# Kernel tuning notes

Hardware: AMD Instinct MI355X
Metric: run time of the kernel (lower is better)

The kernel has to match this reference:

```python
import jax, jax.numpy as jnp
import numpy as np

EMBED = 768
E2 = EMBED // 2  # 384
B = 128
T = 256   # 16x16 search tokens
T1 = 64   # 8x8 template tokens
EPS = 1e-5


def setup_inputs() -> dict:
    key = jax.random.key(0)
    ks = jax.random.split(key, 8)
    s = 0.02
    return {
        "z_r": jax.random.normal(ks[0], (B, T1, EMBED), jnp.float32),
        "z_i": jax.random.normal(ks[1], (B, T1, EMBED), jnp.float32),
        "x_r": jax.random.normal(ks[2], (B, T, EMBED), jnp.float32),
        "x_i": jax.random.normal(ks[3], (B, T, EMBED), jnp.float32),
        "fz_w": jax.random.normal(ks[4], (E2, 2 * EMBED), jnp.float32) * s,
        "fz_b": jnp.zeros((E2,), jnp.float32),
        "ln_g": jnp.ones((E2,), jnp.float32),
        "ln_b": jnp.zeros((E2,), jnp.float32),
        "wr": jax.random.normal(ks[5], (E2, EMBED, 3, 3), jnp.float32) * s,
        "br": jnp.zeros((E2,), jnp.float32),
        "bnr_g": jnp.ones((E2,), jnp.float32),
        "bnr_b": jnp.zeros((E2,), jnp.float32),
        "bnr_m": jnp.zeros((E2,), jnp.float32),
        "bnr_v": jnp.ones((E2,), jnp.float32),
        "wi": jax.random.normal(ks[6], (E2, EMBED, 3, 3), jnp.float32) * s,
        "bi": jnp.zeros((E2,), jnp.float32),
        "bni_g": jnp.ones((E2,), jnp.float32),
        "bni_b": jnp.zeros((E2,), jnp.float32),
        "bni_m": jnp.zeros((E2,), jnp.float32),
        "bni_v": jnp.ones((E2,), jnp.float32),
        "c": jnp.ones((1,), jnp.float32) * E2,
    }


def _gelu(x):
    return jax.nn.gelu(x, approximate=False)


def _layernorm(x, g, b):
    mu = jnp.mean(x, axis=-1, keepdims=True)
    var = jnp.mean(jnp.square(x - mu), axis=-1, keepdims=True)
    return (x - mu) * jax.lax.rsqrt(var + EPS) * g + b


def _conv_bn_gelu(x, w, b, g, beta, m, v):
    # x: [B, C_in, H, W], w: [C_out, C_in, 3, 3]; BN in eval mode (running stats)
    y = jax.lax.conv_general_dilated(
        x, w, window_strides=(1, 1), padding=((1, 1), (1, 1)),
        dimension_numbers=("NCHW", "OIHW", "NCHW"))
    y = y + b[None, :, None, None]
    y = (y - m[None, :, None, None]) * jax.lax.rsqrt(v[None, :, None, None] + EPS)
    y = y * g[None, :, None, None] + beta[None, :, None, None]
    return _gelu(y)


def _xcorr_fast(x, kernel):
    # x: [B, C, H, W]; kernel: [B, C, kh, kw] -> per-sample valid correlation
    def one(xb, kb):
        return jax.lax.conv_general_dilated(
            xb[None], kb[None], window_strides=(1, 1), padding="VALID",
            dimension_numbers=("NCHW", "OIHW", "NCHW"))[0]
    return jax.vmap(one)(x, kernel)  # [B, 1, oh, ow]


def reference(z_r, z_i, x_r, x_i, fz_w, fz_b, ln_g, ln_b,
              wr, br, bnr_g, bnr_b, bnr_m, bnr_v,
              wi, bi, bni_g, bni_b, bni_m, bni_v, c):
    Bn, t, embed = x_r.shape
    t1 = z_r.shape[1]
    sq, sq1 = int(np.sqrt(t)), int(np.sqrt(t1))
    # f_z: Linear + LayerNorm + GELU on concat(z_r, z_i)
    z = jnp.concatenate((z_r, z_i), axis=2)          # [B, t1, 2*embed]
    z = jnp.einsum("bte,oe->bto", z, fz_w) + fz_b    # [B, t1, E2]
    z = _gelu(_layernorm(z, ln_g, ln_b))
    z_f = z.transpose(0, 2, 1).reshape(Bn, -1, sq1, sq1)  # [B, E2, 8, 8]
    # down_r / down_i on search features
    xr = x_r.transpose(0, 2, 1).reshape(Bn, embed, sq, sq)
    xi = x_i.transpose(0, 2, 1).reshape(Bn, embed, sq, sq)
    xr = _conv_bn_gelu(xr, wr, br, bnr_g, bnr_b, bnr_m, bnr_v)
    xi = _conv_bn_gelu(xi, wi, bi, bni_g, bni_b, bni_m, bni_v)
    # center crop 16x16 -> 8x8
    xr = xr[:, :, 4:-4, 4:-4]
    xi = xi[:, :, 4:-4, 4:-4]
    s1 = jax.nn.sigmoid(_xcorr_fast(xr, z_f) / c)
    s2 = jax.nn.sigmoid(_xcorr_fast(xi, z_f) / c)
    return (s1, s2)
```

## Files before the change

### kernel.cpp

```cpp
#include <hip/hip_runtime.h>
#include <hip/hip_bf16.h>
#include <math.h>

#define EPSF 1e-5f

typedef __bf16 v8bf __attribute__((ext_vector_type(8)));
typedef float  v4f  __attribute__((ext_vector_type(4)));
typedef unsigned int u32;
typedef unsigned short u16;

__device__ __forceinline__ float gelu_exact(float x) {
    return 0.5f * x * (1.0f + erff(x * 0.70710678f));
}
__device__ __forceinline__ u16 f2bf(float f) {
    u32 u = __float_as_uint(f);
    return (u16)((u + 0x7fffu + ((u >> 16) & 1u)) >> 16);
}
__device__ __forceinline__ float bf2f(u16 u) {
    return __uint_as_float(((u32)u) << 16);
}
__device__ __forceinline__ void gload16(const void* g, void* l) {
    __builtin_amdgcn_global_load_lds((const __attribute__((address_space(1))) u32*)g,
                                     (__attribute__((address_space(3))) u32*)l, 16, 0, 0);
}

#define BARRIER(N) do { \
    asm volatile("s_waitcnt vmcnt(" #N ") lgkmcnt(0)" ::: "memory"); \
    __builtin_amdgcn_s_barrier(); \
} while (0)

__global__ __launch_bounds__(256) void kprep_z(const float* __restrict__ fz_w,
                                               u16* __restrict__ Bz) {
    int idx = blockIdx.x * 256 + threadIdx.x;
    int n = idx / 192;
    int r = idx % 192;
    int ec2 = r >> 2;
    int h = r & 3;
    const float* src = fz_w + (size_t)n * 1536 + ec2 * 32 + h * 8;
    float4 v0 = *(const float4*)src;
    float4 v1 = *(const float4*)(src + 4);
    uint4 pk;
    pk.x = (u32)f2bf(v0.x) | ((u32)f2bf(v0.y) << 16);
    pk.y = (u32)f2bf(v0.z) | ((u32)f2bf(v0.w) << 16);
    pk.z = (u32)f2bf(v1.x) | ((u32)f2bf(v1.y) << 16);
    pk.w = (u32)f2bf(v1.z) | ((u32)f2bf(v1.w) << 16);
    size_t slot = ((size_t)(ec2 * 4 + h) * 384 + n);
    *(uint4*)(Bz + slot * 8) = pk;
}

__global__ __launch_bounds__(256) void kprep_w(const float* __restrict__ wr,
                                               const float* __restrict__ wi,
                                               u16* __restrict__ Bw) {
    __shared__ float wsm[6912];
    const int tid = threadIdx.x;
    const int n = blockIdx.x >> 1;
    const int conv = blockIdx.x & 1;
    const float* w = (conv ? wi : wr) + (size_t)n * 6912;
#pragma unroll
    for (int k = 0; k < 7; ++k) {
        int sl = tid + k * 256;
        if (sl < 1728) ((float4*)wsm)[sl] = ((const float4*)w)[sl];
    }
    __syncthreads();
#pragma unroll
    for (int k = 0; k < 4; ++k) {
        int sl = tid + k * 256;
        if (sl < 864) {
            int h = sl & 3;
            int r = sl >> 2;
            int ec2 = r % 24;
            int s = r / 24;
            int ch0 = ec2 * 32 + h * 8;
            u16 tmp[8];
#pragma unroll
            for (int e = 0; e < 8; ++e) tmp[e] = f2bf(wsm[(ch0 + e) * 9 + s]);
            uint4 pk;
            pk.x = (u32)tmp[0] | ((u32)tmp[1] << 16);
            pk.y = (u32)tmp[2] | ((u32)tmp[3] << 16);
            pk.z = (u32)tmp[4] | ((u32)tmp[5] << 16);
            pk.w = (u32)tmp[6] | ((u32)tmp[7] << 16);
            size_t slot = ((size_t)conv * 864 + sl) * 384 + n;
            *(uint4*)(Bw + slot * 8) = pk;
        }
    }
}

#define ZB_BUF 24576
#define ZA_BUF 2048

__global__ __launch_bounds__(384, 1) void kz2(const float* __restrict__ z_r,
                                              const float* __restrict__ z_i,
                                              const u16* __restrict__ Bz,
                                              const float* __restrict__ fz_b,
                                              const float* __restrict__ ln_g,
                                              const float* __restrict__ ln_b,
                                              u16* __restrict__ zpk) {
    const int th = blockIdx.x;
    const int b  = blockIdx.y;
    const int tid  = threadIdx.x;
    const int lane = tid & 63;
    const int wid  = tid >> 6;
    const int l15  = lane & 15;
    const int h    = lane >> 4;

    __shared__ __align__(16) char lds[3 * ZB_BUF + 2 * ZA_BUF];
    char* ldsZB = lds;
    char* ldsZA = lds + 3 * ZB_BUF;
    __shared__ float redS[6 * 32], redQ[6 * 32], mu_s[32], rs_s[32];

    const float* zr_b = z_r + (size_t)b * (64 * 768);
    const float* zi_b = z_i + (size_t)b * (64 * 768);

    int boff[4];
#pragma unroll
    for (int nj = 0; nj < 4; ++nj) {
        int n = wid * 64 + nj * 16 + l15;
        boff[nj] = h * 6144 + n * 16;
    }
    int zaoff[2];
#pragma unroll
    for (int mi = 0; mi < 2; ++mi)
        zaoff[mi] = h * 512 + (mi * 16 + l15) * 16;

    auto stageZB = [&](int ec2, char* buf) {
        const char* src = (const char*)(Bz + (size_t)ec2 * 1536 * 8);
#pragma unroll
        for (int k = 0; k < 4; ++k) {
            int sl = tid + k * 384;
            gload16(src + sl * 16, buf + sl * 16);
        }
    };
    auto issueZA = [&](int ec2, float4* zr) {
        const float* zsrc = (ec2 < 24) ? zr_b : zi_b;
        const int ch0 = (ec2 < 24 ? ec2 : ec2 - 24) * 32;
        int sl = tid & 255;
        int row = sl >> 3, qq = sl & 7;
        zr[0] = *(const float4*)(zsrc + (size_t)(th * 32 + row) * 768 + ch0 + qq * 4);
    };
    auto convertZA = [&](const float4* zr, char* buf) {
        int sl = tid & 255;
        int row = sl >> 3, qq = sl & 7;
        ushort4 pk;
        pk.x = f2bf(zr[0].x); pk.y = f2bf(zr[0].y);
        pk.z = f2bf(zr[0].z); pk.w = f2bf(zr[0].w);
        *(ushort4*)(buf + (qq >> 1) * 512 + row * 16 + (qq & 1) * 8) = pk;
    };

    v4f acc[2][4] = {};

    auto comp = [&](char* curA, char* curB) {
        v8bf a[2], bfv[4];
#pragma unroll
        for (int mi = 0; mi < 2; ++mi) a[mi] = *(const v8bf*)(curA + zaoff[mi]);
#pragma unroll
        for (int nj = 0; nj < 4; ++nj) bfv[nj] = *(const v8bf*)(curB + boff[nj]);
        __builtin_amdgcn_s_setprio(1);
#pragma unroll
        for (int mi = 0; mi < 2; ++mi)
#pragma unroll
            for (int nj = 0; nj < 4; ++nj)
                acc[mi][nj] = __builtin_amdgcn_mfma_f32_16x16x32_bf16(a[mi], bfv[nj], acc[mi][nj], 0, 0, 0);
        __builtin_amdgcn_s_setprio(0);
    };

    float4 zreg[1];
    {
        issueZA(0, zreg);
        stageZB(0, ldsZB);
        stageZB(1, ldsZB + ZB_BUF);
        convertZA(zreg, ldsZA);
        issueZA(1, zreg);
        BARRIER(5);
    }
#pragma unroll 1
    for (int t = 0; t < 46; ++t) {
        stageZB(t + 2, ldsZB + ((t + 2) % 3) * ZB_BUF);
        comp(ldsZA + (t & 1) * ZA_BUF, ldsZB + (t % 3) * ZB_BUF);
        convertZA(zreg, ldsZA + ((t + 1) & 1) * ZA_BUF);
        issueZA(t + 2, zreg);
        BARRIER(5);
    }
    {
        comp(ldsZA + (46 & 1) * ZA_BUF, ldsZB + (46 % 3) * ZB_BUF);
        convertZA(zreg, ldsZA + (47 & 1) * ZA_BUF);
        BARRIER(0);
    }
    comp(ldsZA + (47 & 1) * ZA_BUF, ldsZB + (47 % 3) * ZB_BUF);

    float fzb[4], lng[4], lnb[4];
#pragma unroll
    for (int nj = 0; nj < 4; ++nj) {
        int o = wid * 64 + nj * 16 + l15;
        fzb[nj] = fz_b[o]; lng[nj] = ln_g[o]; lnb[nj] = ln_b[o];
    }
#pragma unroll
    for (int mi = 0; mi < 2; ++mi)
#pragma unroll
        for (int nj = 0; nj < 4; ++nj)
#pragma unroll
            for (int reg = 0; reg < 4; ++reg)
                acc[mi][nj][reg] += fzb[nj];

#pragma unroll
    for (int mi = 0; mi < 2; ++mi) {
#pragma unroll
        for (int reg = 0; reg < 4; ++reg) {
            float s = 0.f, q = 0.f;
#pragma unroll
            for (int nj = 0; nj < 4; ++nj) {
                float v = acc[mi][nj][reg];
                s += v; q += v * v;
            }
#pragma unroll
            for (int m = 0; m < 4; ++m) {
                s += __shfl_xor(s, 1 << m, 64);
                q += __shfl_xor(q, 1 << m, 64);
            }
            if (l15 == 0) {
                int row = mi * 16 + h * 4 + reg;
                redS[wid * 32 + row] = s;
                redQ[wid * 32 + row] = q;
            }
        }
    }
    __syncthreads();
    if (tid < 32) {
        float s = 0.f, q = 0.f;
#pragma unroll
        for (int w6 = 0; w6 < 6; ++w6) { s += redS[w6 * 32 + tid]; q += redQ[w6 * 32 + tid]; }
        float mu = s * (1.0f / 384.0f);
        float var = q * (1.0f / 384.0f) - mu * mu;
        mu_s[tid] = mu;
        rs_s[tid] = rsqrtf(var + EPSF);
    }
    __syncthreads();

#pragma unroll
    for (int mi = 0; mi < 2; ++mi)
#pragma unroll
        for (int nj = 0; nj < 4; ++nj) {
            int o = wid * 64 + nj * 16 + l15;
            u32* dst = (u32*)zpk + ((size_t)b * 384 + o) * 32 + th * 16 + mi * 8 + h * 2;
#pragma unroll
            for (int rp = 0; rp < 2; ++rp) {
                float zv[2];
#pragma unroll
                for (int k = 0; k < 2; ++k) {
                    int reg = rp * 2 + k;
                    int row = mi * 16 + h * 4 + reg;
                    float v = (acc[mi][nj][reg] - mu_s[row]) * rs_s[row] * lng[nj] + lnb[nj];
                    zv[k] = gelu_exact(v);
                }
                dst[rp] = (u32)f2bf(zv[0]) | ((u32)f2bf(zv[1]) << 16);
            }
        }
}

#define APL14  2816
#define ABUF14 (4 * APL14)
#define SSTR14 589824
#define ESTR14 24576

__global__ __launch_bounds__(768, 3) void kc14(const float* __restrict__ x_r,
                                               const float* __restrict__ x_i,
                                               const u16* __restrict__ Bw,
                                               const u16* __restrict__ zpk,
                                               const float* __restrict__ br,  const float* __restrict__ bnr_g,
                                               const float* __restrict__ bnr_b, const float* __restrict__ bnr_m,
                                               const float* __restrict__ bnr_v,
                                               const float* __restrict__ bi,  const float* __restrict__ bni_g,
                                               const float* __restrict__ bni_b, const float* __restrict__ bni_m,
                                               const float* __restrict__ bni_v,
                                               float* __restrict__ part) {
    const int conv = blockIdx.x;
    const int b    = blockIdx.y;
    const int tid  = threadIdx.x;
    const int lane = tid & 63;
    const int wid  = tid >> 6;
    const int l15  = lane & 15;
    const int h    = lane >> 4;

    __shared__ __align__(16) char ldsA[2 * ABUF14];
    __shared__ float redF[12];

    const float* x  = conv ? x_i : x_r;
    const float* xb = x + (size_t)b * (256 * 768);

    const char* bbase = (const char*)(Bw + (size_t)conv * (864 * 384 * 8))
                      + (size_t)h * 6144 + (wid * 32 + l15) * 16;

    int aoff[4];
#pragma unroll
    for (int mi = 0; mi < 4; ++mi) {
        int p = mi * 16 + l15;
        int i = p >> 3, j = p & 7;
        aoff[mi] = h * APL14 + (i * 16 + j + 3) * 16;
    }

    auto issueA = [&](int ec2, float4* ar) {
#pragma unroll
        for (int k = 0; k < 2; ++k) {
            int sl = tid + k * 768;
            if (sl >= 1408) sl -= 1408;
            int row = sl >> 3, qq = sl & 7;
            ar[k] = *(const float4*)(xb + (size_t)(48 + row) * 768 + ec2 * 32 + qq * 4);
        }
    };
    auto convertA = [&](const float4* ar, char* buf) {
#pragma unroll
        for (int k = 0; k < 2; ++k) {
            int sl = tid + k * 768;
            if (sl >= 1408) sl -= 1408;
            int row = sl >> 3, qq = sl & 7;
            ushort4 pk;
            pk.x = f2bf(ar[k].x); pk.y = f2bf(ar[k].y);
            pk.z = f2bf(ar[k].z); pk.w = f2bf(ar[k].w);
            *(ushort4*)(buf + (qq >> 1) * APL14 + row * 16 + (qq & 1) * 8) = pk;
        }
    };

    v4f acc[4][2] = {};
    v8bf bpipe[3][2];
    float4 areg[2];

    {
        issueA(0, areg);
#pragma unroll
        for (int i = 0; i < 3; ++i) {
            const char* p = bbase + (size_t)i * SSTR14;
            bpipe[i][0] = *(const v8bf*)p;
            bpipe[i][1] = *(const v8bf*)(p + 256);
        }
        convertA(areg, ldsA);
        BARRIER(6);
    }

#define TAP(S) do { \
        v8bf b0 = bpipe[(S) % 3][0]; \
        v8bf b1 = bpipe[(S) % 3][1]; \
        const int _so = (((S) / 3) * 16 + ((S) % 3)) * 16; \
        v8bf a0 = *(const v8bf*)(Acur + aoff[0] + _so); \
        v8bf a1 = *(const v8bf*)(Acur + aoff[1] + _so); \
        v8bf a2 = *(const v8bf*)(Acur + aoff[2] + _so); \
        v8bf a3 = *(const v8bf*)(Acur + aoff[3] + _so); \
        __builtin_amdgcn_s_setprio(1); \
        acc[0][0] = __builtin_amdgcn_mfma_f32_16x16x32_bf16(a0, b0, acc[0][0], 0, 0, 0); \
        acc[0][1] = __builtin_amdgcn_mfma_f32_16x16x32_bf16(a0, b1, acc[0][1], 0, 0, 0); \
        acc[1][0] = __builtin_amdgcn_mfma_f32_16x16x32_bf16(a1, b0, acc[1][0], 0, 0, 0); \
        acc[1][1] = __builtin_amdgcn_mfma_f32_16x16x32_bf16(a1, b1, acc[1][1], 0, 0, 0); \
        acc[2][0] = __builtin_amdgcn_mfma_f32_16x16x32_bf16(a2, b0, acc[2][0], 0, 0, 0); \
        acc[2][1] = __builtin_amdgcn_mfma_f32_16x16x32_bf16(a2, b1, acc[2][1], 0, 0, 0); \
        acc[3][0] = __builtin_amdgcn_mfma_f32_16x16x32_bf16(a3, b0, acc[3][0], 0, 0, 0); \
        acc[3][1] = __builtin_amdgcn_mfma_f32_16x16x32_bf16(a3, b1, acc[3][1], 0, 0, 0); \
        __builtin_amdgcn_s_setprio(0); \
        if ((S) <= 5) { \
            const char* _p = bptr + (size_t)((S) + 3) * SSTR14; \
            bpipe[(S) % 3][0] = *(const v8bf*)_p; \
            bpipe[(S) % 3][1] = *(const v8bf*)(_p + 256); \
        } else if (e < 23) { \
            const char* _p = bptr + ESTR14 + (size_t)((S) - 6) * SSTR14; \
            bpipe[(S) % 3][0] = *(const v8bf*)_p; \
            bpipe[(S) % 3][1] = *(const v8bf*)(_p + 256); \
        } \
    } while (0)

#pragma unroll 1
    for (int e = 0; e < 24; ++e) {
        const char* Acur = ldsA + (e & 1) * ABUF14;
        const char* bptr = bbase + (size_t)e * ESTR14;
        TAP(0); TAP(1); TAP(2);
        if (e < 23) issueA(e + 1, areg);
        TAP(3); TAP(4); TAP(5); TAP(6);
        if (e < 23) convertA(areg, ldsA + ((e + 1) & 1) * ABUF14);
        TAP(7); TAP(8);
        if (e < 23) BARRIER(6);
    }
#undef TAP

    const float* bcp = conv ? bi    : br;
    const float* gp  = conv ? bni_g : bnr_g;
    const float* bbp = conv ? bni_b : bnr_b;
    const float* mp  = conv ? bni_m : bnr_m;
    const float* vp  = conv ? bni_v : bnr_v;

    float sum = 0.f;
#pragma unroll
    for (int nj = 0; nj < 2; ++nj) {
        const int o = wid * 32 + nj * 16 + l15;
        const float sc  = gp[o] * rsqrtf(vp[o] + EPSF);
        const float sh2 = (bcp[o] - mp[o]) * sc + bbp[o];
        const u16* zb = zpk + ((size_t)b * 384 + o) * 64;
#pragma unroll
        for (int mi = 0; mi < 4; ++mi) {
            ushort4 zw = *(const ushort4*)(zb + mi * 16 + h * 4);
#pragma unroll
            for (int reg = 0; reg < 4; ++reg) {
                float y = fmaf(acc[mi][nj][reg], sc, sh2);
                u16 zu = (reg == 0) ? zw.x : (reg == 1) ? zw.y : (reg == 2) ? zw.z : zw.w;
                sum = fmaf(gelu_exact(y), bf2f(zu), sum);
            }
        }
    }
#pragma unroll
    for (int off = 32; off >= 1; off >>= 1) sum += __shfl_down(sum, off, 64);

    if (lane == 0) redF[wid] = sum;
    __syncthreads();
    if (tid == 0) {
        float t = 0.f;
#pragma unroll
        for (int w12 = 0; w12 < 12; ++w12) t += redF[w12];
        part[(size_t)conv * 128 + b] = t;
    }
}

__global__ __launch_bounds__(256) void kr(const float* __restrict__ part,
                                          const float* __restrict__ c,
                                          float* __restrict__ out) {
    int v = threadIdx.x;
    out[v] = 1.f / (1.f + expf(-part[v] / c[0]));
}

extern "C" void kernel_launch(void* const* d_in, const int* in_sizes, int n_in,
                              void* d_out, int out_size, void* d_ws, size_t ws_size,
                              hipStream_t stream) {
    const float* z_r   = (const float*)d_in[0];
    const float* z_i   = (const float*)d_in[1];
    const float* x_r   = (const float*)d_in[2];
    const float* x_i   = (const float*)d_in[3];
    const float* fz_w  = (const float*)d_in[4];
    const float* fz_b  = (const float*)d_in[5];
    const float* ln_g  = (const float*)d_in[6];
    const float* ln_b  = (const float*)d_in[7];
    const float* wr    = (const float*)d_in[8];
    const float* br    = (const float*)d_in[9];
    const float* bnr_g = (const float*)d_in[10];
    const float* bnr_b = (const float*)d_in[11];
    const float* bnr_m = (const float*)d_in[12];
    const float* bnr_v = (const float*)d_in[13];
    const float* wi    = (const float*)d_in[14];
    const float* bi    = (const float*)d_in[15];
    const float* bni_g = (const float*)d_in[16];
    const float* bni_b = (const float*)d_in[17];
    const float* bni_m = (const float*)d_in[18];
    const float* bni_v = (const float*)d_in[19];
    const float* c     = (const float*)d_in[20];

    u16*   Bz   = (u16*)d_ws;
    u16*   Bw   = (u16*)((char*)d_ws + 1179648);
    u16*   zpk  = (u16*)((char*)d_ws + 1179648 + 10616832);
    float* part = (float*)((char*)d_ws + 1179648 + 10616832 + 6291456);

    kprep_z<<<288, 256, 0, stream>>>(fz_w, Bz);
    kprep_w<<<768, 256, 0, stream>>>(wr, wi, Bw);
    kz2<<<dim3(2, 128), 384, 0, stream>>>(z_r, z_i, Bz, fz_b, ln_g, ln_b, zpk);
    kc14<<<dim3(2, 128), 768, 0, stream>>>(x_r, x_i, Bw, zpk,
                                           br, bnr_g, bnr_b, bnr_m, bnr_v,
                                           bi, bni_g, bni_b, bni_m, bni_v,
                                           part);
    kr<<<1, 256, 0, stream>>>(part, c, (float*)d_out);
}
```

Baseline: 163.9 us.

## Split conv K loop across two wave groups with wider N tiles per wave

The conv kernel now splits its 12 waves into two groups that each take alternate 32-channel input slabs (split-K), while each wave covers 64 output channels instead of 32. The A slabs for both groups are loaded per iteration, which halves the loop count and the barrier count and gives each A fragment read from LDS twice as many MFMAs. Partial accumulators are combined through LDS at the end, and only group 0 runs the epilogue. This doubles accumulator and B-pipeline register use, which risks spills or lower occupancy, and adds an LDS reduction step.

```diff
diff --git a/kernel.cpp b/kernel.cpp
--- a/kernel.cpp
+++ b/kernel.cpp
@@ -256,12 +256,12 @@
         }
 }
 
-#define APL14  2816
-#define ABUF14 (4 * APL14)
-#define SSTR14 589824
-#define ESTR14 24576
-
-__global__ __launch_bounds__(768, 3) void kc14(const float* __restrict__ x_r,
+#define APL15  2816
+#define SLAB15 (4 * APL15)
+#define SSTR15 589824
+#define ESTR15 24576
+
+__global__ __launch_bounds__(768, 3) void kc15(const float* __restrict__ x_r,
                                                const float* __restrict__ x_i,
                                                const u16* __restrict__ Bw,
                                                const u16* __restrict__ zpk,
@@ -277,140 +277,180 @@
     const int tid  = threadIdx.x;
     const int lane = tid & 63;
     const int wid  = tid >> 6;
+    const int g    = (wid >= 6) ? 1 : 0;
+    const int cg   = wid - g * 6;
     const int l15  = lane & 15;
     const int h    = lane >> 4;
 
-    __shared__ __align__(16) char ldsA[2 * ABUF14];
+    __shared__ __align__(16) char ldsA[4 * SLAB15];
     __shared__ float redF[12];
 
     const float* x  = conv ? x_i : x_r;
     const float* xb = x + (size_t)b * (256 * 768);
 
     const char* bbase = (const char*)(Bw + (size_t)conv * (864 * 384 * 8))
-                      + (size_t)h * 6144 + (wid * 32 + l15) * 16;
+                      + (size_t)h * 6144 + (cg * 64 + l15) * 16;
 
     int aoff[4];
 #pragma unroll
     for (int mi = 0; mi < 4; ++mi) {
         int p = mi * 16 + l15;
         int i = p >> 3, j = p & 7;
-        aoff[mi] = h * APL14 + (i * 16 + j + 3) * 16;
-    }
-
-    auto issueA = [&](int ec2, float4* ar) {
-#pragma unroll
-        for (int k = 0; k < 2; ++k) {
+        aoff[mi] = h * APL15 + (i * 16 + j + 3) * 16;
+    }
+
+    auto issueA = [&](int eBase, float4* ar) {
+#pragma unroll
+        for (int k = 0; k < 4; ++k) {
             int sl = tid + k * 768;
-            if (sl >= 1408) sl -= 1408;
-            int row = sl >> 3, qq = sl & 7;
-            ar[k] = *(const float4*)(xb + (size_t)(48 + row) * 768 + ec2 * 32 + qq * 4);
+            if (sl >= 2816) sl -= 2816;
+            int par = (sl >= 1408) ? 1 : 0;
+            int r2 = sl - par * 1408;
+            int row = r2 >> 3, qq = r2 & 7;
+            ar[k] = *(const float4*)(xb + (size_t)(48 + row) * 768 + (eBase + par) * 32 + qq * 4);
         }
     };
-    auto convertA = [&](const float4* ar, char* buf) {
-#pragma unroll
-        for (int k = 0; k < 2; ++k) {
+    auto convertA = [&](const float4* ar, char* bufBase) {
+#pragma unroll
+        for (int k = 0; k < 4; ++k) {
             int sl = tid + k * 768;
-            if (sl >= 1408) sl -= 1408;
-            int row = sl >> 3, qq = sl & 7;
+            if (sl >= 2816) sl -= 2816;
+            int par = (sl >= 1408) ? 1 : 0;
+            int r2 = sl - par * 1408;
+            int row = r2 >> 3, qq = r2 & 7;
             ushort4 pk;
             pk.x = f2bf(ar[k].x); pk.y = f2bf(ar[k].y);
             pk.z = f2bf(ar[k].z); pk.w = f2bf(ar[k].w);
-            *(ushort4*)(buf + (qq >> 1) * APL14 + row * 16 + (qq & 1) * 8) = pk;
+            *(ushort4*)(bufBase + par * SLAB15 + (qq >> 1) * APL15 + row * 16 + (qq & 1) * 8) = pk;
         }
     };
 
-    v4f acc[4][2] = {};
-    v8bf bpipe[3][2];
-    float4 areg[2];
+    v4f acc[4][4] = {};
+    v8bf bpipe[3][4];
+    float4 areg[4];
 
     {
         issueA(0, areg);
 #pragma unroll
         for (int i = 0; i < 3; ++i) {
-            const char* p = bbase + (size_t)i * SSTR14;
-            bpipe[i][0] = *(const v8bf*)p;
-            bpipe[i][1] = *(const v8bf*)(p + 256);
+            const char* p = bbase + (size_t)g * ESTR15 + (size_t)i * SSTR15;
+#pragma unroll
+            for (int nj = 0; nj < 4; ++nj)
+                bpipe[i][nj] = *(const v8bf*)(p + nj * 256);
         }
         convertA(areg, ldsA);
-        BARRIER(6);
+        BARRIER(12);
     }
 
 #define TAP(S) do { \
-        v8bf b0 = bpipe[(S) % 3][0]; \
-        v8bf b1 = bpipe[(S) % 3][1]; \
         const int _so = (((S) / 3) * 16 + ((S) % 3)) * 16; \
         v8bf a0 = *(const v8bf*)(Acur + aoff[0] + _so); \
         v8bf a1 = *(const v8bf*)(Acur + aoff[1] + _so); \
         v8bf a2 = *(const v8bf*)(Acur + aoff[2] + _so); \
         v8bf a3 = *(const v8bf*)(Acur + aoff[3] + _so); \
         __builtin_amdgcn_s_setprio(1); \
-        acc[0][0] = __builtin_amdgcn_mfma_f32_16x16x32_bf16(a0, b0, acc[0][0], 0, 0, 0); \
-        acc[0][1] = __builtin_amdgcn_mfma_f32_16x16x32_bf16(a0, b1, acc[0][1], 0, 0, 0); \
-        acc[1][0] = __builtin_amdgcn_mfma_f32_16x16x32_bf16(a1, b0, acc[1][0], 0, 0, 0); \
-        acc[1][1] = __builtin_amdgcn_mfma_f32_16x16x32_bf16(a1, b1, acc[1][1], 0, 0, 0); \
-        acc[2][0] = __builtin_amdgcn_mfma_f32_16x16x32_bf16(a2, b0, acc[2][0], 0, 0, 0); \
-        acc[2][1] = __builtin_amdgcn_mfma_f32_16x16x32_bf16(a2, b1, acc[2][1], 0, 0, 0); \
-        acc[3][0] = __builtin_amdgcn_mfma_f32_16x16x32_bf16(a3, b0, acc[3][0], 0, 0, 0); \
-        acc[3][1] = __builtin_amdgcn_mfma_f32_16x16x32_bf16(a3, b1, acc[3][1], 0, 0, 0); \
+        acc[0][0] = __builtin_amdgcn_mfma_f32_16x16x32_bf16(a0, bpipe[(S) % 3][0], acc[0][0], 0, 0, 0); \
+        acc[0][1] = __builtin_amdgcn_mfma_f32_16x16x32_bf16(a0, bpipe[(S) % 3][1], acc[0][1], 0, 0, 0); \
+        acc[0][2] = __builtin_amdgcn_mfma_f32_16x16x32_bf16(a0, bpipe[(S) % 3][2], acc[0][2], 0, 0, 0); \
+        acc[0][3] = __builtin_amdgcn_mfma_f32_16x16x32_bf16(a0, bpipe[(S) % 3][3], acc[0][3], 0, 0, 0); \
+        acc[1][0] = __builtin_amdgcn_mfma_f32_16x16x32_bf16(a1, bpipe[(S) % 3][0], acc[1][0], 0, 0, 0); \
+        acc[1][1] = __builtin_amdgcn_mfma_f32_16x16x32_bf16(a1, bpipe[(S) % 3][1], acc[1][1], 0, 0, 0); \
+        acc[1][2] = __builtin_amdgcn_mfma_f32_16x16x32_bf16(a1, bpipe[(S) % 3][2], acc[1][2], 0, 0, 0); \
+        acc[1][3] = __builtin_amdgcn_mfma_f32_16x16x32_bf16(a1, bpipe[(S) % 3][3], acc[1][3], 0, 0, 0); \
+        acc[2][0] = __builtin_amdgcn_mfma_f32_16x16x32_bf16(a2, bpipe[(S) % 3][0], acc[2][0], 0, 0, 0); \
+        acc[2][1] = __builtin_amdgcn_mfma_f32_16x16x32_bf16(a2, bpipe[(S) % 3][1], acc[2][1], 0, 0, 0); \
+        acc[2][2] = __builtin_amdgcn_mfma_f32_16x16x32_bf16(a2, bpipe[(S) % 3][2], acc[2][2], 0, 0, 0); \
+        acc[2][3] = __builtin_amdgcn_mfma_f32_16x16x32_bf16(a2, bpipe[(S) % 3][3], acc[2][3], 0, 0, 0); \
+        acc[3][0] = __builtin_amdgcn_mfma_f32_16x16x32_bf16(a3, bpipe[(S) % 3][0], acc[3][0], 0, 0, 0); \
+        acc[3][1] = __builtin_amdgcn_mfma_f32_16x16x32_bf16(a3, bpipe[(S) % 3][1], acc[3][1], 0, 0, 0); \
+        acc[3][2] = __builtin_amdgcn_mfma_f32_16x16x32_bf16(a3, bpipe[(S) % 3][2], acc[3][2], 0, 0, 0); \
+        acc[3][3] = __builtin_amdgcn_mfma_f32_16x16x32_bf16(a3, bpipe[(S) % 3][3], acc[3][3], 0, 0, 0); \
         __builtin_amdgcn_s_setprio(0); \
         if ((S) <= 5) { \
-            const char* _p = bptr + (size_t)((S) + 3) * SSTR14; \
+            const char* _p = bptr + (size_t)((S) + 3) * SSTR15; \
             bpipe[(S) % 3][0] = *(const v8bf*)_p; \
             bpipe[(S) % 3][1] = *(const v8bf*)(_p + 256); \
-        } else if (e < 23) { \
-            const char* _p = bptr + ESTR14 + (size_t)((S) - 6) * SSTR14; \
+            bpipe[(S) % 3][2] = *(const v8bf*)(_p + 512); \
+            bpipe[(S) % 3][3] = *(const v8bf*)(_p + 768); \
+        } else if (t < 11) { \
+            const char* _p = bptr + 2 * ESTR15 + (size_t)((S) - 6) * SSTR15; \
             bpipe[(S) % 3][0] = *(const v8bf*)_p; \
             bpipe[(S) % 3][1] = *(const v8bf*)(_p + 256); \
+            bpipe[(S) % 3][2] = *(const v8bf*)(_p + 512); \
+            bpipe[(S) % 3][3] = *(const v8bf*)(_p + 768); \
         } \
     } while (0)
 
 #pragma unroll 1
-    for (int e = 0; e < 24; ++e) {
-        const char* Acur = ldsA + (e & 1) * ABUF14;
-        const char* bptr = bbase + (size_t)e * ESTR14;
+    for (int t = 0; t < 12; ++t) {
+        const char* Acur = ldsA + ((t & 1) * 2 + g) * SLAB15;
+        const char* bptr = bbase + (size_t)(2 * t + g) * ESTR15;
         TAP(0); TAP(1); TAP(2);
-        if (e < 23) issueA(e + 1, areg);
+        if (t < 11) issueA(2 * t + 2, areg);
         TAP(3); TAP(4); TAP(5); TAP(6);
-        if (e < 23) convertA(areg, ldsA + ((e + 1) & 1) * ABUF14);
+        if (t < 11) convertA(areg, ldsA + (((t + 1) & 1) * 2) * SLAB15);
         TAP(7); TAP(8);
-        if (e < 23) BARRIER(6);
+        if (t < 11) BARRIER(12);
     }
 #undef TAP
 
-    const float* bcp = conv ? bi    : br;
-    const float* gp  = conv ? bni_g : bnr_g;
-    const float* bbp = conv ? bni_b : bnr_b;
-    const float* mp  = conv ? bni_m : bnr_m;
-    const float* vp  = conv ? bni_v : bnr_v;
+    __syncthreads();
+    float* P = (float*)ldsA;
+#pragma unroll
+    for (int mi = 0; mi < 4; ++mi) {
+        if (g == 1) {
+#pragma unroll
+            for (int nj = 0; nj < 4; ++nj)
+#pragma unroll
+                for (int reg = 0; reg < 4; ++reg)
+                    P[(((nj * 4 + reg) * 6 + cg) * 64) + lane] = acc[mi][nj][reg];
+        }
+        __syncthreads();
+        if (g == 0) {
+#pragma unroll
+            for (int nj = 0; nj < 4; ++nj)
+#pragma unroll
+                for (int reg = 0; reg < 4; ++reg)
+                    acc[mi][nj][reg] += P[(((nj * 4 + reg) * 6 + cg) * 64) + lane];
+        }
+        __syncthreads();
+    }
 
     float sum = 0.f;
-#pragma unroll
-    for (int nj = 0; nj < 2; ++nj) {
-        const int o = wid * 32 + nj * 16 + l15;
-        const float sc  = gp[o] * rsqrtf(vp[o] + EPSF);
-        const float sh2 = (bcp[o] - mp[o]) * sc + bbp[o];
-        const u16* zb = zpk + ((size_t)b * 384 + o) * 64;
-#pragma unroll
-        for (int mi = 0; mi < 4; ++mi) {
-            ushort4 zw = *(const ushort4*)(zb + mi * 16 + h * 4);
-#pragma unroll
-            for (int reg = 0; reg < 4; ++reg) {
-                float y = fmaf(acc[mi][nj][reg], sc, sh2);
-                u16 zu = (reg == 0) ? zw.x : (reg == 1) ? zw.y : (reg == 2) ? zw.z : zw.w;
-                sum = fmaf(gelu_exact(y), bf2f(zu), sum);
+    if (g == 0) {
+        const float* bcp = conv ? bi    : br;
+        const float* gp  = conv ? bni_g : bnr_g;
+        const float* bbp = conv ? bni_b : bnr_b;
+        const float* mp  = conv ? bni_m : bnr_m;
+        const float* vp  = conv ? bni_v : bnr_v;
+#pragma unroll
+        for (int nj = 0; nj < 4; ++nj) {
+            const int o = cg * 64 + nj * 16 + l15;
+            const float sc  = gp[o] * rsqrtf(vp[o] + EPSF);
+            const float sh2 = (bcp[o] - mp[o]) * sc + bbp[o];
+            const u16* zb = zpk + ((size_t)b * 384 + o) * 64;
+#pragma unroll
+            for (int mi = 0; mi < 4; ++mi) {
+                ushort4 zw = *(const ushort4*)(zb + mi * 16 + h * 4);
+#pragma unroll
+                for (int reg = 0; reg < 4; ++reg) {
+                    float y = fmaf(acc[mi][nj][reg], sc, sh2);
+                    u16 zu = (reg == 0) ? zw.x : (reg == 1) ? zw.y : (reg == 2) ? zw.z : zw.w;
+                    sum = fmaf(gelu_exact(y), bf2f(zu), sum);
+                }
             }
         }
-    }
-#pragma unroll
-    for (int off = 32; off >= 1; off >>= 1) sum += __shfl_down(sum, off, 64);
-
-    if (lane == 0) redF[wid] = sum;
+#pragma unroll
+        for (int off = 32; off >= 1; off >>= 1) sum += __shfl_down(sum, off, 64);
+    }
+
+    if (lane == 0) redF[wid] = (g == 0) ? sum : 0.f;
     __syncthreads();
     if (tid == 0) {
-        float t = 0.f;
-#pragma unroll
-        for (int w12 = 0; w12 < 12; ++w12) t += redF[w12];
-        part[(size_t)conv * 128 + b] = t;
+        float tt = 0.f;
+#pragma unroll
+        for (int w12 = 0; w12 < 12; ++w12) tt += redF[w12];
+        part[(size_t)conv * 128 + b] = tt;
     }
 }
 
@@ -454,7 +494,7 @@
     kprep_z<<<288, 256, 0, stream>>>(fz_w, Bz);
     kprep_w<<<768, 256, 0, stream>>>(wr, wi, Bw);
     kz2<<<dim3(2, 128), 384, 0, stream>>>(z_r, z_i, Bz, fz_b, ln_g, ln_b, zpk);
-    kc14<<<dim3(2, 128), 768, 0, stream>>>(x_r, x_i, Bw, zpk,
+    kc15<<<dim3(2, 128), 768, 0, stream>>>(x_r, x_i, Bw, zpk,
                                            br, bnr_g, bnr_b, bnr_m, bnr_v,
                                            bi, bni_g, bni_b, bni_m, bni_v,
                                            part);
```

New measurement: 245.9 us. 50.0% more time.

## Split conv blocks by output-row halves with wider per-wave channel tiles

Applied to the files above, without the earlier changes.

The conv+xcorr kernel now launches four blocks per batch item, so each (conv, half of the cropped rows) pair gets its own block. Each block has 6 waves, and each wave covers 64 output channels over 32 positions instead of 32 channels over 64 positions. Each block stages a smaller input slab in LDS, and the two partial sums are combined in the final sigmoid kernel. This doubles the grid for better CU occupancy and load balance, but every weight tile is now read by twice as many blocks and each thread holds more B-pipeline registers.

```diff
diff --git a/kernel.cpp b/kernel.cpp
--- a/kernel.cpp
+++ b/kernel.cpp
@@ -256,12 +256,12 @@
         }
 }
 
-#define APL14  2816
-#define ABUF14 (4 * APL14)
-#define SSTR14 589824
-#define ESTR14 24576
-
-__global__ __launch_bounds__(768, 3) void kc14(const float* __restrict__ x_r,
+#define APL16  1536
+#define ABUF16 (4 * APL16)
+#define SSTR16 589824
+#define ESTR16 24576
+
+__global__ __launch_bounds__(384, 3) void kc16(const float* __restrict__ x_r,
                                                const float* __restrict__ x_i,
                                                const u16* __restrict__ Bw,
                                                const u16* __restrict__ zpk,
@@ -272,7 +272,9 @@
                                                const float* __restrict__ bni_b, const float* __restrict__ bni_m,
                                                const float* __restrict__ bni_v,
                                                float* __restrict__ part) {
-    const int conv = blockIdx.x;
+    const int q    = blockIdx.x;
+    const int conv = q >> 1;
+    const int mh   = q & 1;
     const int b    = blockIdx.y;
     const int tid  = threadIdx.x;
     const int lane = tid & 63;
@@ -280,100 +282,99 @@
     const int l15  = lane & 15;
     const int h    = lane >> 4;
 
-    __shared__ __align__(16) char ldsA[2 * ABUF14];
-    __shared__ float redF[12];
+    __shared__ __align__(16) char ldsA[2 * ABUF16];
+    __shared__ float redF[6];
 
     const float* x  = conv ? x_i : x_r;
     const float* xb = x + (size_t)b * (256 * 768);
 
     const char* bbase = (const char*)(Bw + (size_t)conv * (864 * 384 * 8))
-                      + (size_t)h * 6144 + (wid * 32 + l15) * 16;
-
-    int aoff[4];
-#pragma unroll
-    for (int mi = 0; mi < 4; ++mi) {
+                      + (size_t)h * 6144 + (wid * 64 + l15) * 16;
+
+    int aoff[2];
+#pragma unroll
+    for (int mi = 0; mi < 2; ++mi) {
         int p = mi * 16 + l15;
-        int i = p >> 3, j = p & 7;
-        aoff[mi] = h * APL14 + (i * 16 + j + 3) * 16;
+        int li = p >> 3, j = p & 7;
+        aoff[mi] = h * APL16 + (li * 16 + j + 3) * 16;
     }
 
     auto issueA = [&](int ec2, float4* ar) {
 #pragma unroll
         for (int k = 0; k < 2; ++k) {
-            int sl = tid + k * 768;
-            if (sl >= 1408) sl -= 1408;
+            int sl = tid + k * 384;
             int row = sl >> 3, qq = sl & 7;
-            ar[k] = *(const float4*)(xb + (size_t)(48 + row) * 768 + ec2 * 32 + qq * 4);
+            ar[k] = *(const float4*)(xb + (size_t)(48 + mh * 64 + row) * 768 + ec2 * 32 + qq * 4);
         }
     };
     auto convertA = [&](const float4* ar, char* buf) {
 #pragma unroll
         for (int k = 0; k < 2; ++k) {
-            int sl = tid + k * 768;
-            if (sl >= 1408) sl -= 1408;
+            int sl = tid + k * 384;
             int row = sl >> 3, qq = sl & 7;
             ushort4 pk;
             pk.x = f2bf(ar[k].x); pk.y = f2bf(ar[k].y);
             pk.z = f2bf(ar[k].z); pk.w = f2bf(ar[k].w);
-            *(ushort4*)(buf + (qq >> 1) * APL14 + row * 16 + (qq & 1) * 8) = pk;
-        }
-    };
-
-    v4f acc[4][2] = {};
-    v8bf bpipe[3][2];
+            *(ushort4*)(buf + (qq >> 1) * APL16 + row * 16 + (qq & 1) * 8) = pk;
+        }
+    };
+
+    v4f acc[2][4] = {};
+    v8bf bpipe[3][4];
     float4 areg[2];
 
     {
         issueA(0, areg);
 #pragma unroll
         for (int i = 0; i < 3; ++i) {
-            const char* p = bbase + (size_t)i * SSTR14;
-            bpipe[i][0] = *(const v8bf*)p;
-            bpipe[i][1] = *(const v8bf*)(p + 256);
+            const char* p = bbase + (size_t)i * SSTR16;
+#pragma unroll
+            for (int nj = 0; nj < 4; ++nj)
+                bpipe[i][nj] = *(const v8bf*)(p + nj * 256);
         }
         convertA(areg, ldsA);
-        BARRIER(6);
+        BARRIER(12);
     }
 
 #define TAP(S) do { \
-        v8bf b0 = bpipe[(S) % 3][0]; \
-        v8bf b1 = bpipe[(S) % 3][1]; \
         const int _so = (((S) / 3) * 16 + ((S) % 3)) * 16; \
         v8bf a0 = *(const v8bf*)(Acur + aoff[0] + _so); \
         v8bf a1 = *(const v8bf*)(Acur + aoff[1] + _so); \
-        v8bf a2 = *(const v8bf*)(Acur + aoff[2] + _so); \
-        v8bf a3 = *(const v8bf*)(Acur + aoff[3] + _so); \
         __builtin_amdgcn_s_setprio(1); \
-        acc[0][0] = __builtin_amdgcn_mfma_f32_16x16x32_bf16(a0, b0, acc[0][0], 0, 0, 0); \
-        acc[0][1] = __builtin_amdgcn_mfma_f32_16x16x32_bf16(a0, b1, acc[0][1], 0, 0, 0); \
-        acc[1][0] = __builtin_amdgcn_mfma_f32_16x16x32_bf16(a1, b0, acc[1][0], 0, 0, 0); \
-        acc[1][1] = __builtin_amdgcn_mfma_f32_16x16x32_bf16(a1, b1, acc[1][1], 0, 0, 0); \
-        acc[2][0] = __builtin_amdgcn_mfma_f32_16x16x32_bf16(a2, b0, acc[2][0], 0, 0, 0); \
-        acc[2][1] = __builtin_amdgcn_mfma_f32_16x16x32_bf16(a2, b1, acc[2][1], 0, 0, 0); \
-        acc[3][0] = __builtin_amdgcn_mfma_f32_16x16x32_bf16(a3, b0, acc[3][0], 0, 0, 0); \
-        acc[3][1] = __builtin_amdgcn_mfma_f32_16x16x32_bf16(a3, b1, acc[3][1], 0, 0, 0); \
+        acc[0][0] = __builtin_amdgcn_mfma_f32_16x16x32_bf16(a0, bpipe[(S) % 3][0], acc[0][0], 0, 0, 0); \
+        acc[0][1] = __builtin_amdgcn_mfma_f32_16x16x32_bf16(a0, bpipe[(S) % 3][1], acc[0][1], 0, 0, 0); \
+        acc[0][2] = __builtin_amdgcn_mfma_f32_16x16x32_bf16(a0, bpipe[(S) % 3][2], acc[0][2], 0, 0, 0); \
+        acc[0][3] = __builtin_amdgcn_mfma_f32_16x16x32_bf16(a0, bpipe[(S) % 3][3], acc[0][3], 0, 0, 0); \
+        acc[1][0] = __builtin_amdgcn_mfma_f32_16x16x32_bf16(a1, bpipe[(S) % 3][0], acc[1][0], 0, 0, 0); \
+        acc[1][1] = __builtin_amdgcn_mfma_f32_16x16x32_bf16(a1, bpipe[(S) % 3][1], acc[1][1], 0, 0, 0); \
+        acc[1][2] = __builtin_amdgcn_mfma_f32_16x16x32_bf16(a1, bpipe[(S) % 3][2], acc[1][2], 0, 0, 0); \
+        acc[1][3] = __builtin_amdgcn_mfma_f32_16x16x32_bf16(a1, bpipe[(S) % 3][3], acc[1][3], 0, 0, 0); \
         __builtin_amdgcn_s_setprio(0); \
         if ((S) <= 5) { \
-            const char* _p = bptr + (size_t)((S) + 3) * SSTR14; \
+            const char* _p = bptr + (size_t)((S) + 3) * SSTR16; \
             bpipe[(S) % 3][0] = *(const v8bf*)_p; \
             bpipe[(S) % 3][1] = *(const v8bf*)(_p + 256); \
+            bpipe[(S) % 3][2] = *(const v8bf*)(_p + 512); \
+            bpipe[(S) % 3][3] = *(const v8bf*)(_p + 768); \
         } else if (e < 23) { \
-            const char* _p = bptr + ESTR14 + (size_t)((S) - 6) * SSTR14; \
+            const char* _p = bptr + ESTR16 + (size_t)((S) - 6) * SSTR16; \
             bpipe[(S) % 3][0] = *(const v8bf*)_p; \
             bpipe[(S) % 3][1] = *(const v8bf*)(_p + 256); \
+            bpipe[(S) % 3][2] = *(const v8bf*)(_p + 512); \
+            bpipe[(S) % 3][3] = *(const v8bf*)(_p + 768); \
         } \
     } while (0)
 
 #pragma unroll 1
     for (int e = 0; e < 24; ++e) {
-        const char* Acur = ldsA + (e & 1) * ABUF14;
-        const char* bptr = bbase + (size_t)e * ESTR14;
+        const char* Acur = ldsA + (e & 1) * ABUF16;
+        const char* bptr = bbase + (size_t)e * ESTR16;
         TAP(0); TAP(1); TAP(2);
         if (e < 23) issueA(e + 1, areg);
         TAP(3); TAP(4); TAP(5); TAP(6);
-        if (e < 23) convertA(areg, ldsA + ((e + 1) & 1) * ABUF14);
+        if (e < 23) convertA(areg, ldsA + ((e + 1) & 1) * ABUF16);
         TAP(7); TAP(8);
-        if (e < 23) BARRIER(6);
+        if (e < 23) BARRIER(12);
     }
 #undef TAP
 
@@ -385,14 +386,14 @@
 
     float sum = 0.f;
 #pragma unroll
-    for (int nj = 0; nj < 2; ++nj) {
-        const int o = wid * 32 + nj * 16 + l15;
+    for (int nj = 0; nj < 4; ++nj) {
+        const int o = wid * 64 + nj * 16 + l15;
         const float sc  = gp[o] * rsqrtf(vp[o] + EPSF);
         const float sh2 = (bcp[o] - mp[o]) * sc + bbp[o];
         const u16* zb = zpk + ((size_t)b * 384 + o) * 64;
 #pragma unroll
-        for (int mi = 0; mi < 4; ++mi) {
-            ushort4 zw = *(const ushort4*)(zb + mi * 16 + h * 4);
+        for (int mi = 0; mi < 2; ++mi) {
+            ushort4 zw = *(const ushort4*)(zb + mh * 32 + mi * 16 + h * 4);
 #pragma unroll
             for (int reg = 0; reg < 4; ++reg) {
                 float y = fmaf(acc[mi][nj][reg], sc, sh2);
@@ -407,10 +408,8 @@
     if (lane == 0) redF[wid] = sum;
     __syncthreads();
     if (tid == 0) {
-        float t = 0.f;
-#pragma unroll
-        for (int w12 = 0; w12 < 12; ++w12) t += redF[w12];
-        part[(size_t)conv * 128 + b] = t;
+        float t = redF[0] + redF[1] + redF[2] + redF[3] + redF[4] + redF[5];
+        part[((size_t)conv * 128 + b) * 2 + mh] = t;
     }
 }
 
@@ -418,7 +417,8 @@
                                           const float* __restrict__ c,
                                           float* __restrict__ out) {
     int v = threadIdx.x;
-    out[v] = 1.f / (1.f + expf(-part[v] / c[0]));
+    float s = part[v * 2] + part[v * 2 + 1];
+    out[v] = 1.f / (1.f + expf(-s / c[0]));
 }
 
 extern "C" void kernel_launch(void* const* d_in, const int* in_sizes, int n_in,
@@ -454,7 +454,7 @@
     kprep_z<<<288, 256, 0, stream>>>(fz_w, Bz);
     kprep_w<<<768, 256, 0, stream>>>(wr, wi, Bw);
     kz2<<<dim3(2, 128), 384, 0, stream>>>(z_r, z_i, Bz, fz_b, ln_g, ln_b, zpk);
-    kc14<<<dim3(2, 128), 768, 0, stream>>>(x_r, x_i, Bw, zpk,
+    kc16<<<dim3(4, 128), 384, 0, stream>>>(x_r, x_i, Bw, zpk,
                                            br, bnr_g, bnr_b, bnr_m, bnr_v,
                                            bi, bni_g, bni_b, bni_m, bni_v,
                                            part);
```

Result: slower. 203.3 us (+24.0%).

## Split conv K-dimension across two blocks and fuse epilogue into separate reduction kernel

Applied to the files above, without the earlier changes.

The conv kernel now splits the 24 input-channel chunks into two halves, launching 512 blocks instead of 256, and writes bf16 partial conv outputs to workspace. A new epilogue kernel sums the two partials, applies BN+GELU, correlates with the template features and applies the sigmoid, replacing the old final kernel. This targets poor CU occupancy from only 256 large blocks, at the cost of extra global traffic for partials and bf16 rounding of the partial sums.

```diff
diff --git a/kernel.cpp b/kernel.cpp
--- a/kernel.cpp
+++ b/kernel.cpp
@@ -261,27 +261,22 @@
 #define SSTR14 589824
 #define ESTR14 24576
 
-__global__ __launch_bounds__(768, 3) void kc14(const float* __restrict__ x_r,
+__global__ __launch_bounds__(768, 6) void kc17(const float* __restrict__ x_r,
                                                const float* __restrict__ x_i,
                                                const u16* __restrict__ Bw,
-                                               const u16* __restrict__ zpk,
-                                               const float* __restrict__ br,  const float* __restrict__ bnr_g,
-                                               const float* __restrict__ bnr_b, const float* __restrict__ bnr_m,
-                                               const float* __restrict__ bnr_v,
-                                               const float* __restrict__ bi,  const float* __restrict__ bni_g,
-                                               const float* __restrict__ bni_b, const float* __restrict__ bni_m,
-                                               const float* __restrict__ bni_v,
-                                               float* __restrict__ part) {
-    const int conv = blockIdx.x;
+                                               u16* __restrict__ P) {
+    const int q    = blockIdx.x;
+    const int kh   = q >> 1;
+    const int conv = q & 1;
     const int b    = blockIdx.y;
     const int tid  = threadIdx.x;
     const int lane = tid & 63;
     const int wid  = tid >> 6;
     const int l15  = lane & 15;
     const int h    = lane >> 4;
+    const int e0   = kh * 12;
 
     __shared__ __align__(16) char ldsA[2 * ABUF14];
-    __shared__ float redF[12];
 
     const float* x  = conv ? x_i : x_r;
     const float* xb = x + (size_t)b * (256 * 768);
@@ -324,10 +319,10 @@
     float4 areg[2];
 
     {
-        issueA(0, areg);
+        issueA(e0, areg);
 #pragma unroll
         for (int i = 0; i < 3; ++i) {
-            const char* p = bbase + (size_t)i * SSTR14;
+            const char* p = bbase + (size_t)e0 * ESTR14 + (size_t)i * SSTR14;
             bpipe[i][0] = *(const v8bf*)p;
             bpipe[i][1] = *(const v8bf*)(p + 256);
         }
@@ -357,7 +352,7 @@
             const char* _p = bptr + (size_t)((S) + 3) * SSTR14; \
             bpipe[(S) % 3][0] = *(const v8bf*)_p; \
             bpipe[(S) % 3][1] = *(const v8bf*)(_p + 256); \
-        } else if (e < 23) { \
+        } else if (e < e0 + 11) { \
             const char* _p = bptr + ESTR14 + (size_t)((S) - 6) * SSTR14; \
             bpipe[(S) % 3][0] = *(const v8bf*)_p; \
             bpipe[(S) % 3][1] = *(const v8bf*)(_p + 256); \
@@ -365,17 +360,46 @@
     } while (0)
 
 #pragma unroll 1
-    for (int e = 0; e < 24; ++e) {
+    for (int e = e0; e < e0 + 12; ++e) {
         const char* Acur = ldsA + (e & 1) * ABUF14;
         const char* bptr = bbase + (size_t)e * ESTR14;
         TAP(0); TAP(1); TAP(2);
-        if (e < 23) issueA(e + 1, areg);
+        if (e < e0 + 11) issueA(e + 1, areg);
         TAP(3); TAP(4); TAP(5); TAP(6);
-        if (e < 23) convertA(areg, ldsA + ((e + 1) & 1) * ABUF14);
+        if (e < e0 + 11) convertA(areg, ldsA + ((e + 1) & 1) * ABUF14);
         TAP(7); TAP(8);
-        if (e < 23) BARRIER(6);
+        if (e < e0 + 11) BARRIER(6);
     }
 #undef TAP
+
+    u16* Pd = P + ((size_t)(q * 128 + b)) * 24576;
+#pragma unroll
+    for (int nj = 0; nj < 2; ++nj) {
+        const int o = wid * 32 + nj * 16 + l15;
+#pragma unroll
+        for (int mi = 0; mi < 4; ++mi) {
+#pragma unroll
+            for (int reg = 0; reg < 4; ++reg) {
+                int pix = mi * 16 + h * 4 + reg;
+                Pd[pix * 384 + o] = f2bf(acc[mi][nj][reg]);
+            }
+        }
+    }
+}
+
+__global__ __launch_bounds__(384) void ke(const u16* __restrict__ P,
+                                          const u16* __restrict__ zpk,
+                                          const float* __restrict__ br,  const float* __restrict__ bnr_g,
+                                          const float* __restrict__ bnr_b, const float* __restrict__ bnr_m,
+                                          const float* __restrict__ bnr_v,
+                                          const float* __restrict__ bi,  const float* __restrict__ bni_g,
+                                          const float* __restrict__ bni_b, const float* __restrict__ bni_m,
+                                          const float* __restrict__ bni_v,
+                                          const float* __restrict__ c,
+                                          float* __restrict__ out) {
+    const int b = blockIdx.x;
+    const int conv = blockIdx.y;
+    const int o = threadIdx.x;
 
     const float* bcp = conv ? bi    : br;
     const float* gp  = conv ? bni_g : bnr_g;
@@ -383,42 +407,31 @@
     const float* mp  = conv ? bni_m : bnr_m;
     const float* vp  = conv ? bni_v : bnr_v;
 
+    const float sc = gp[o] * rsqrtf(vp[o] + EPSF);
+    const float sh = (bcp[o] - mp[o]) * sc + bbp[o];
+
+    const u16* P0 = P + ((size_t)((0 * 2 + conv) * 128 + b)) * 24576 + o;
+    const u16* P1 = P + ((size_t)((1 * 2 + conv) * 128 + b)) * 24576 + o;
+    const u16* zb = zpk + ((size_t)b * 384 + o) * 64;
+
     float sum = 0.f;
-#pragma unroll
-    for (int nj = 0; nj < 2; ++nj) {
-        const int o = wid * 32 + nj * 16 + l15;
-        const float sc  = gp[o] * rsqrtf(vp[o] + EPSF);
-        const float sh2 = (bcp[o] - mp[o]) * sc + bbp[o];
-        const u16* zb = zpk + ((size_t)b * 384 + o) * 64;
-#pragma unroll
-        for (int mi = 0; mi < 4; ++mi) {
-            ushort4 zw = *(const ushort4*)(zb + mi * 16 + h * 4);
-#pragma unroll
-            for (int reg = 0; reg < 4; ++reg) {
-                float y = fmaf(acc[mi][nj][reg], sc, sh2);
-                u16 zu = (reg == 0) ? zw.x : (reg == 1) ? zw.y : (reg == 2) ? zw.z : zw.w;
-                sum = fmaf(gelu_exact(y), bf2f(zu), sum);
-            }
-        }
-    }
+#pragma unroll 4
+    for (int pix = 0; pix < 64; ++pix) {
+        float cv = bf2f(P0[pix * 384]) + bf2f(P1[pix * 384]);
+        float y = fmaf(cv, sc, sh);
+        sum = fmaf(gelu_exact(y), bf2f(zb[pix]), sum);
+    }
+
+    __shared__ float red[6];
 #pragma unroll
     for (int off = 32; off >= 1; off >>= 1) sum += __shfl_down(sum, off, 64);
-
-    if (lane == 0) redF[wid] = sum;
+    const int wv = o >> 6, ln = o & 63;
+    if (ln == 0) red[wv] = sum;
     __syncthreads();
-    if (tid == 0) {
-        float t = 0.f;
-#pragma unroll
-        for (int w12 = 0; w12 < 12; ++w12) t += redF[w12];
-        part[(size_t)conv * 128 + b] = t;
-    }
-}
-
-__global__ __launch_bounds__(256) void kr(const float* __restrict__ part,
-                                          const float* __restrict__ c,
-                                          float* __restrict__ out) {
-    int v = threadIdx.x;
-    out[v] = 1.f / (1.f + expf(-part[v] / c[0]));
+    if (o == 0) {
+        float t = red[0] + red[1] + red[2] + red[3] + red[4] + red[5];
+        out[conv * 128 + b] = 1.f / (1.f + expf(-t / c[0]));
+    }
 }
 
 extern "C" void kernel_launch(void* const* d_in, const int* in_sizes, int n_in,
@@ -446,17 +459,17 @@
     const float* bni_v = (const float*)d_in[19];
     const float* c     = (const float*)d_in[20];
 
-    u16*   Bz   = (u16*)d_ws;
-    u16*   Bw   = (u16*)((char*)d_ws + 1179648);
-    u16*   zpk  = (u16*)((char*)d_ws + 1179648 + 10616832);
-    float* part = (float*)((char*)d_ws + 1179648 + 10616832 + 6291456);
+    u16* Bz  = (u16*)d_ws;
+    u16* Bw  = (u16*)((char*)d_ws + 1179648);
+    u16* zpk = (u16*)((char*)d_ws + 1179648 + 10616832);
+    u16* P   = (u16*)((char*)d_ws + 1179648 + 10616832 + 6291456);
 
     kprep_z<<<288, 256, 0, stream>>>(fz_w, Bz);
     kprep_w<<<768, 256, 0, stream>>>(wr, wi, Bw);
     kz2<<<dim3(2, 128), 384, 0, stream>>>(z_r, z_i, Bz, fz_b, ln_g, ln_b, zpk);
-    kc14<<<dim3(2, 128), 768, 0, stream>>>(x_r, x_i, Bw, zpk,
-                                           br, bnr_g, bnr_b, bnr_m, bnr_v,
-                                           bi, bni_g, bni_b, bni_m, bni_v,
-                                           part);
-    kr<<<1, 256, 0, stream>>>(part, c, (float*)d_out);
-}
+    kc17<<<dim3(4, 128), 768, 0, stream>>>(x_r, x_i, Bw, P);
+    ke<<<dim3(128, 2), 384, 0, stream>>>(P, zpk,
+                                         br, bnr_g, bnr_b, bnr_m, bnr_v,
+                                         bi, bni_g, bni_b, bni_m, bni_v,
+                                         c, (float*)d_out);
+}
```

New measurement: 292.0 us. +78.1%, slower.
